# Optimization experiments

Hardware: AMD Instinct MI355X
Metric: run time of the kernel (lower is better)

The kernel has to match this reference:

```python
import jax, jax.numpy as jnp
import numpy as np

TEMPERATURE = 0.07
EPS = 1e-8


def setup_inputs() -> dict:
    key = jax.random.key(0)
    k1, k2 = jax.random.split(key)
    B, D = 8192, 256
    embeddings = jax.random.normal(k1, (B, D), dtype=jnp.float32)
    labels = jax.random.randint(k2, (B,), 0, 6, dtype=jnp.int64)
    return {"embeddings": embeddings, "labels": labels}


def reference(embeddings, labels):
    B = embeddings.shape[0]
    # F.normalize(p=2, dim=1): x / max(||x||, eps)
    norm = jnp.linalg.norm(embeddings, axis=1, keepdims=True)
    en = embeddings / jnp.maximum(norm, 1e-12)
    sim = en @ en.T  # [B, B]
    s = sim / TEMPERATURE

    eye = jnp.eye(B, dtype=bool)
    same = labels[:, None] == labels[None, :]
    pos_mask = same & ~eye            # [B, B]
    neg_mask = (~same) & ~eye         # [B, B]

    exp_s = jnp.exp(s)
    # per-row sum of exp over negatives (matches inner-loop denominator term)
    neg_sum = jnp.sum(jnp.where(neg_mask, exp_s, 0.0), axis=1)  # [B]

    # rows contribute only if they have >=1 positive AND >=1 negative
    row_valid = (pos_mask.sum(axis=1) > 0) & (neg_mask.sum(axis=1) > 0)
    pair_mask = pos_mask & row_valid[:, None]

    # -log( exp(s_ij) / (exp(s_ij) + neg_sum_i + 1e-8) ) per positive pair
    per_pair = -jnp.log(exp_s / (exp_s + neg_sum[:, None] + EPS))
    total = jnp.sum(jnp.where(pair_mask, per_pair, 0.0))
    count = jnp.sum(pair_mask)
    loss = jnp.where(count > 0, total / jnp.maximum(count, 1).astype(total.dtype), 0.0)
    return loss
```

## Files before the change

### kernel.cpp

```cpp
#include <hip/hip_runtime.h>
#include <hip/hip_bf16.h>

#define B_ 8192
#define D_ 256
#define TINV 14.285714285714285f
#define EPS_ 1e-8f
#define BK 32
#define NBLK 32
#define NT 64
#define NTRI (NT*(NT+1)/2)

typedef short short8 __attribute__((ext_vector_type(8)));
typedef float f32x4 __attribute__((ext_vector_type(4)));

__device__ __forceinline__ void mfma_bf16(f32x4& acc, short8 a, short8 b) {
    asm("v_mfma_f32_16x16x32_bf16 %0, %1, %2, %0" : "+v"(acc) : "v"(a), "v"(b));
}

__device__ __forceinline__ void mfma_fence() {
    __builtin_amdgcn_sched_barrier(0);
    asm volatile("s_nop 7\ns_nop 7" ::);
}

__device__ __forceinline__ unsigned short f2bf(float x) {
    __hip_bfloat16 h = __float2bfloat16(x);
    return __builtin_bit_cast(unsigned short, h);
}

__device__ __forceinline__ void tri_decode(int idx, int& bi, int& bj) {
    int t = NTRI - 1 - idx;
    int u = (int)((sqrtf(8.f * (float)t + 1.f) - 1.f) * 0.5f);
    while (u * (u + 1) / 2 > t) --u;
    while ((u + 1) * (u + 2) / 2 <= t) ++u;
    bi = (NT - 1) - u;
    bj = (NT - 1) - (t - u * (u + 1) / 2);
}

__device__ __forceinline__ void stage(const char* gbase, int row0, int k0,
                                      short* ldst, int lane, int wid) {
    int p = (wid << 6) + lane;
    int row = p >> 2;
    int kb = (p & 3) ^ ((row >> 1) & 3);
    const char* g = gbase + ((size_t)(row0 + row) * (D_ * 2) + (size_t)(k0 + kb * 8) * 2);
    __builtin_amdgcn_global_load_lds(
        (const __attribute__((address_space(1))) unsigned int*)g,
        (__attribute__((address_space(3))) unsigned int*)(ldst + ((size_t)wid << 9)),
        16, 0, 0);
}

__device__ __forceinline__ void compute_step(const short* lA, const short* lB,
                                             int lane, int wm, int wn, f32x4 acc[2][4]) {
    int rl = lane & 15, kb = lane >> 4;
    short8 a[2];
#pragma unroll
    for (int m = 0; m < 2; ++m) {
        int row = wm * 32 + m * 16 + rl;
        a[m] = ((const short8*)lA)[row * 4 + (kb ^ ((row >> 1) & 3))];
    }
#pragma unroll
    for (int n = 0; n < 4; ++n) {
        int row = wn * 64 + n * 16 + rl;
        short8 b = ((const short8*)lB)[row * 4 + (kb ^ ((row >> 1) & 3))];
        mfma_bf16(acc[0][n], a[0], b);
        mfma_bf16(acc[1][n], a[1], b);
    }
}

__device__ __forceinline__ void gemm_pipe(const char* enb, int i0, int j0,
                                          short (*lA)[128 * BK], short (*lB)[128 * BK],
                                          int lane, int wid, int wm, int wn,
                                          f32x4 acc[2][4]) {
    stage(enb, i0, 0, lA[0], lane, wid);
    stage(enb, j0, 0, lB[0], lane, wid);
    stage(enb, i0, BK, lA[1], lane, wid);
    stage(enb, j0, BK, lB[1], lane, wid);
#define PIPE_STEP(T, WAITS)                                                     \
    {                                                                           \
        asm volatile(WAITS ::: "memory");                                       \
        __builtin_amdgcn_sched_barrier(0);                                      \
        __builtin_amdgcn_s_barrier();                                           \
        __builtin_amdgcn_sched_barrier(0);                                      \
        if ((T) + 2 < 8) {                                                      \
            stage(enb, i0, ((T) + 2) * BK, lA[((T) + 2) % 3], lane, wid);       \
            stage(enb, j0, ((T) + 2) * BK, lB[((T) + 2) % 3], lane, wid);       \
        }                                                                       \
        compute_step(lA[(T) % 3], lB[(T) % 3], lane, wm, wn, acc);              \
    }
    PIPE_STEP(0, "s_waitcnt vmcnt(2)")
    PIPE_STEP(1, "s_waitcnt vmcnt(2)")
    PIPE_STEP(2, "s_waitcnt vmcnt(2)")
    PIPE_STEP(3, "s_waitcnt vmcnt(2)")
    PIPE_STEP(4, "s_waitcnt vmcnt(2)")
    PIPE_STEP(5, "s_waitcnt vmcnt(2)")
    PIPE_STEP(6, "s_waitcnt vmcnt(2)")
    PIPE_STEP(7, "s_waitcnt vmcnt(0)")
#undef PIPE_STEP
    mfma_fence();
}

__global__ __launch_bounds__(256) void k_bhist(const int* __restrict__ labels,
                                               unsigned* __restrict__ blockhist,
                                               float* __restrict__ negsum,
                                               float* __restrict__ total) {
    __shared__ unsigned h[8];
    int b = blockIdx.x, t = threadIdx.x;
    if (t < 8) h[t] = 0;
    negsum[b * 256 + t] = 0.f;
    if (b == 0 && t == 0) *total = 0.f;
    __syncthreads();
    atomicAdd(&h[labels[b * 256 + t] & 7], 1u);
    __syncthreads();
    if (t < 8) blockhist[b * 8 + t] = h[t];
}

__global__ __launch_bounds__(256) void k_pos(const int* __restrict__ labels,
                                             const unsigned* __restrict__ blockhist,
                                             unsigned* __restrict__ hist,
                                             int* __restrict__ pos) {
    __shared__ unsigned cnt[8][NBLK];
    __shared__ unsigned clsbase[8];
    __shared__ unsigned wcnt[4][8];
    int b = blockIdx.x, t = threadIdx.x;
    { int bb = t >> 3, c = t & 7; cnt[c][bb] = blockhist[bb * 8 + c]; }
    __syncthreads();
    if (t < 8) {
        unsigned run = 0;
        for (int b2 = 0; b2 < NBLK; ++b2) {
            unsigned v = cnt[t][b2];
            cnt[t][b2] = run;
            run += v;
        }
        clsbase[t] = run;
        if (b == 0) hist[t] = run;
    }
    __syncthreads();
    if (t == 0) {
        unsigned run = 0;
        for (int c = 0; c < 8; ++c) {
            unsigned tot = clsbase[c];
            clsbase[c] = run;
            run += tot;
        }
    }
    __syncthreads();
    int row = b * 256 + t;
    int c = labels[row] & 7;
    int lane = t & 63, w = t >> 6;
    unsigned long long lanebelow = (1ull << lane) - 1ull;
    unsigned myrank = 0;
#pragma unroll
    for (int cv = 0; cv < 8; ++cv) {
        unsigned long long mask = __ballot(c == cv);
        if (lane == 0) wcnt[w][cv] = (unsigned)__popcll(mask);
        if (c == cv) myrank = (unsigned)__popcll(mask & lanebelow);
    }
    __syncthreads();
    unsigned pre = 0;
    for (int wp = 0; wp < 4; ++wp) if (wp < w) pre += wcnt[wp][c];
    pos[row] = (int)(clsbase[c] + cnt[c][b] + pre + myrank);
}

__global__ __launch_bounds__(256) void k_scatter(const float* __restrict__ emb,
                                                 const int* __restrict__ labels,
                                                 const int* __restrict__ pos,
                                                 __hip_bfloat16* __restrict__ en_s,
                                                 int* __restrict__ lab_s) {
    int row = blockIdx.x * 4 + (threadIdx.x >> 6);
    int lane = threadIdx.x & 63;
    float4 v = reinterpret_cast<const float4*>(emb)[(size_t)row * 64 + lane];
    float ss = v.x * v.x + v.y * v.y + v.z * v.z + v.w * v.w;
#pragma unroll
    for (int off = 32; off >= 1; off >>= 1) ss += __shfl_xor(ss, off, 64);
    float scale = 1.0f / fmaxf(sqrtf(ss), 1e-12f);
    int p = pos[row];
    ushort4 o;
    o.x = f2bf(v.x * scale);
    o.y = f2bf(v.y * scale);
    o.z = f2bf(v.z * scale);
    o.w = f2bf(v.w * scale);
    reinterpret_cast<ushort4*>(en_s)[(size_t)p * 64 + lane] = o;
    if (lane == 0) lab_s[p] = labels[row] & 7;
}

template <bool USEP>
__global__ __launch_bounds__(512, 8) void k_negsum(const __hip_bfloat16* __restrict__ en,
                                                   const int* __restrict__ lab_s,
                                                   float* __restrict__ P,
                                                   float* __restrict__ negsum) {
    __shared__ short lA[3][128 * BK];
    __shared__ short lB[3][128 * BK];
    __shared__ int sLi[128], sLj[128];
    int bi, bj;
    tri_decode(blockIdx.x, bi, bj);
    int i0 = bi * 128, j0 = bj * 128;
    int tid = threadIdx.x;
    if (tid < 128) sLi[tid] = lab_s[i0 + tid];
    else if (tid < 256) sLj[tid - 128] = lab_s[j0 + tid - 128];
    __syncthreads();

    int lane = tid & 63, wid = tid >> 6;
    int wm = wid >> 1, wn = wid & 1;
    f32x4 acc[2][4] = {};
    gemm_pipe((const char*)en, i0, j0, lA, lB, lane, wid, wm, wn, acc);

    int rl = lane & 15, rowg = (lane >> 4) * 4;
    int lj[4], li[2][4];
#pragma unroll
    for (int n = 0; n < 4; ++n) lj[n] = sLj[wn * 64 + n * 16 + rl];
#pragma unroll
    for (int m = 0; m < 2; ++m)
#pragma unroll
        for (int r = 0; r < 4; ++r) li[m][r] = sLi[wm * 32 + m * 16 + rowg + r];

    float* sredR = (float*)lA;
    float* sredC = (float*)lB;

    float cp[4] = {0.f, 0.f, 0.f, 0.f};
#pragma unroll
    for (int m = 0; m < 2; ++m) {
        float part[4];
#pragma unroll
        for (int r = 0; r < 4; ++r) {
            part[r] = 0.f;
#pragma unroll
            for (int n = 0; n < 4; ++n) {
                float e = (li[m][r] != lj[n]) ? __expf(acc[m][n][r] * TINV) : 0.f;
                part[r] += e;
                cp[n] += e;
            }
        }
#pragma unroll
        for (int off = 1; off < 16; off <<= 1)
#pragma unroll
            for (int r = 0; r < 4; ++r) part[r] += __shfl_xor(part[r], off, 64);
        if (rl == 0) {
#pragma unroll
            for (int r = 0; r < 4; ++r) {
                int row = wm * 32 + m * 16 + rowg + r;
                if (USEP) sredR[wn * 128 + row] = part[r];
                else      atomicAdd(&negsum[i0 + row], part[r]);
            }
        }
    }
    if (bi != bj) {
#pragma unroll
        for (int n = 0; n < 4; ++n) {
            cp[n] += __shfl_xor(cp[n], 16, 64);
            cp[n] += __shfl_xor(cp[n], 32, 64);
            if (lane < 16) {
                int col = wn * 64 + n * 16 + lane;
                if (USEP) sredC[wm * 128 + col] = cp[n];
                else      atomicAdd(&negsum[j0 + col], cp[n]);
            }
        }
    }
    if (USEP) {
        __syncthreads();
        if (tid < 128)
            P[(size_t)bj * B_ + i0 + tid] = sredR[tid] + sredR[128 + tid];
        else if (tid < 256 && bi != bj) {
            int c = tid - 128;
            P[(size_t)bi * B_ + j0 + c] =
                sredC[c] + sredC[128 + c] + sredC[256 + c] + sredC[384 + c];
        }
    }
}

__global__ __launch_bounds__(256) void k_red(const float* __restrict__ P,
                                             float* __restrict__ negsum) {
    int i = blockIdx.x * 256 + threadIdx.x;
    float s = 0.f;
#pragma unroll 8
    for (int k = 0; k < 64; ++k) s += P[(size_t)k * B_ + i];
    negsum[i] = s;
}

__global__ __launch_bounds__(512, 8) void k_pairs(const __hip_bfloat16* __restrict__ en,
                                                  const int* __restrict__ lab_s,
                                                  const float* __restrict__ negsum,
                                                  const unsigned* __restrict__ hist,
                                                  float* __restrict__ total) {
    int bi, bj;
    tri_decode(blockIdx.x, bi, bj);
    int i0 = bi * 128, j0 = bj * 128;
    if (lab_s[j0] > lab_s[i0 + 127]) return;

    __shared__ short lA[3][128 * BK];
    __shared__ short lB[3][128 * BK];
    __shared__ int sLi[128], sLj[128];
    __shared__ float sNgI[128], sNgJ[128];
    int tid = threadIdx.x;
    if (tid < 128) {
        int l = lab_s[i0 + tid];
        unsigned h = hist[l];
        sLi[tid] = (h > 1u && h < (unsigned)B_) ? l : -1;
        sNgI[tid] = negsum[i0 + tid] + EPS_;
    } else if (tid < 256) {
        int idx = tid - 128;
        int l = lab_s[j0 + idx];
        unsigned h = hist[l];
        sLj[idx] = (h > 1u && h < (unsigned)B_) ? l : -1;
        sNgJ[idx] = negsum[j0 + idx] + EPS_;
    }
    __syncthreads();

    int lane = tid & 63, wid = tid >> 6;
    int wm = wid >> 1, wn = wid & 1;
    f32x4 acc[2][4] = {};
    gemm_pipe((const char*)en, i0, j0, lA, lB, lane, wid, wm, wn, acc);

    int rl = lane & 15, rowg = (lane >> 4) * 4;
    int lj[4];
    float ngJ[4];
#pragma unroll
    for (int n = 0; n < 4; ++n) {
        lj[n] = sLj[wn * 64 + n * 16 + rl];
        ngJ[n] = sNgJ[wn * 64 + n * 16 + rl];
    }

    bool offd = (bi != bj);
    float tot = 0.f;
#pragma unroll
    for (int m = 0; m < 2; ++m) {
#pragma unroll
        for (int r = 0; r < 4; ++r) {
            int ii = wm * 32 + m * 16 + rowg + r;
            int li = sLi[ii];
            float ngI = sNgI[ii];
#pragma unroll
            for (int n = 0; n < 4; ++n) {
                int jj = wn * 64 + n * 16 + rl;
                bool use = (li == lj[n]) && (li >= 0) && (offd || ii != jj);
                if (use) {
                    float s = acc[m][n][r] * TINV;
                    float e = __expf(s);
                    float t = __logf(e + ngI) - s;
                    if (offd) t += __logf(e + ngJ[n]) - s;
                    tot += t;
                }
            }
        }
    }
#pragma unroll
    for (int off = 32; off >= 1; off >>= 1) tot += __shfl_xor(tot, off, 64);
    __shared__ float sred[8];
    if (lane == 0) sred[wid] = tot;
    __syncthreads();
    if (tid == 0) {
        float s = 0.f;
#pragma unroll
        for (int w = 0; w < 8; ++w) s += sred[w];
        atomicAdd(total, s);
    }
}

__global__ __launch_bounds__(64) void k_final(const unsigned* __restrict__ hist,
                                              const float* __restrict__ total,
                                              float* __restrict__ out) {
    int t = threadIdx.x;
    unsigned c = 0;
    if (t < 8) {
        unsigned h = hist[t];
        if (h > 1u && h < (unsigned)B_) c = h * (h - 1u);
    }
#pragma unroll
    for (int off = 4; off >= 1; off >>= 1) c += (unsigned)__shfl_xor((int)c, off, 64);
    if (t == 0) out[0] = (c > 0u) ? total[0] / (float)c : 0.f;
}

extern "C" void kernel_launch(void* const* d_in, const int* in_sizes, int n_in,
                              void* d_out, int out_size, void* d_ws, size_t ws_size,
                              hipStream_t stream) {
    const float* emb = (const float*)d_in[0];
    const int* labels = (const int*)d_in[1];
    float* out = (float*)d_out;
    char* ws = (char*)d_ws;

    const size_t EN_BYTES = (size_t)B_ * D_ * 2;
    __hip_bfloat16* en_s = (__hip_bfloat16*)ws;
    char* p = ws + EN_BYTES;
    float* negsum = (float*)p;            p += (size_t)B_ * 4;
    int* lab_s = (int*)p;                 p += (size_t)B_ * 4;
    int* pos = (int*)p;                   p += (size_t)B_ * 4;
    unsigned* blockhist = (unsigned*)p;   p += NBLK * 8 * 4;
    unsigned* hist = (unsigned*)p;        p += 64;
    float* total = (float*)p;             p += 64;
    float* P = (float*)p;
    size_t need = (size_t)(p - ws) + (size_t)NT * B_ * 4;
    bool bigws = ws_size >= need;

    k_bhist<<<NBLK, 256, 0, stream>>>(labels, blockhist, negsum, total);
    k_pos<<<NBLK, 256, 0, stream>>>(labels, blockhist, hist, pos);
    k_scatter<<<B_ / 4, 256, 0, stream>>>(emb, labels, pos, en_s, lab_s);
    if (bigws) {
        k_negsum<true><<<NTRI, 512, 0, stream>>>(en_s, lab_s, P, negsum);
        k_red<<<B_ / 256, 256, 0, stream>>>(P, negsum);
    } else {
        k_negsum<false><<<NTRI, 512, 0, stream>>>(en_s, lab_s, P, negsum);
    }
    k_pairs<<<NTRI, 512, 0, stream>>>(en_s, lab_s, negsum, hist, total);
    k_final<<<1, 64, 0, stream>>>(hist, total, out);
}
```

Measured before the change: 73.12 us.

## Use atomic negsum accumulation, drop partial buffer and reduction kernel

Removes the per-tile partial-sum buffer P and the separate k_red reduction kernel, so k_negsum always accumulates row and column negative sums into negsum with global atomicAdd. The label staging through shared memory and its __syncthreads are removed; labels are now loaded straight from global memory and those loads are placed before the last pipeline step to hide their latency. This saves one kernel launch, the P round trip and a block barrier, but adds atomic contention on negsum and makes the float summation order nondeterministic.

```diff
diff --git a/kernel.cpp b/kernel.cpp
--- a/kernel.cpp
+++ b/kernel.cpp
@@ -66,14 +66,6 @@
     }
 }
 
-__device__ __forceinline__ void gemm_pipe(const char* enb, int i0, int j0,
-                                          short (*lA)[128 * BK], short (*lB)[128 * BK],
-                                          int lane, int wid, int wm, int wn,
-                                          f32x4 acc[2][4]) {
-    stage(enb, i0, 0, lA[0], lane, wid);
-    stage(enb, j0, 0, lB[0], lane, wid);
-    stage(enb, i0, BK, lA[1], lane, wid);
-    stage(enb, j0, BK, lB[1], lane, wid);
 #define PIPE_STEP(T, WAITS)                                                     \
     {                                                                           \
         asm volatile(WAITS ::: "memory");                                       \
@@ -86,6 +78,15 @@
         }                                                                       \
         compute_step(lA[(T) % 3], lB[(T) % 3], lane, wm, wn, acc);              \
     }
+
+__device__ __forceinline__ void gemm_pipe(const char* enb, int i0, int j0,
+                                          short (*lA)[128 * BK], short (*lB)[128 * BK],
+                                          int lane, int wid, int wm, int wn,
+                                          f32x4 acc[2][4]) {
+    stage(enb, i0, 0, lA[0], lane, wid);
+    stage(enb, j0, 0, lB[0], lane, wid);
+    stage(enb, i0, BK, lA[1], lane, wid);
+    stage(enb, j0, BK, lB[1], lane, wid);
     PIPE_STEP(0, "s_waitcnt vmcnt(2)")
     PIPE_STEP(1, "s_waitcnt vmcnt(2)")
     PIPE_STEP(2, "s_waitcnt vmcnt(2)")
@@ -94,7 +95,6 @@
     PIPE_STEP(5, "s_waitcnt vmcnt(2)")
     PIPE_STEP(6, "s_waitcnt vmcnt(2)")
     PIPE_STEP(7, "s_waitcnt vmcnt(0)")
-#undef PIPE_STEP
     mfma_fence();
 }
 
@@ -182,38 +182,41 @@
     if (lane == 0) lab_s[p] = labels[row] & 7;
 }
 
-template <bool USEP>
 __global__ __launch_bounds__(512, 8) void k_negsum(const __hip_bfloat16* __restrict__ en,
                                                    const int* __restrict__ lab_s,
-                                                   float* __restrict__ P,
                                                    float* __restrict__ negsum) {
     __shared__ short lA[3][128 * BK];
     __shared__ short lB[3][128 * BK];
-    __shared__ int sLi[128], sLj[128];
     int bi, bj;
     tri_decode(blockIdx.x, bi, bj);
     int i0 = bi * 128, j0 = bj * 128;
     int tid = threadIdx.x;
-    if (tid < 128) sLi[tid] = lab_s[i0 + tid];
-    else if (tid < 256) sLj[tid - 128] = lab_s[j0 + tid - 128];
-    __syncthreads();
-
     int lane = tid & 63, wid = tid >> 6;
     int wm = wid >> 1, wn = wid & 1;
+    int rl = lane & 15, rowg = (lane >> 4) * 4;
+    const char* enb = (const char*)en;
+
     f32x4 acc[2][4] = {};
-    gemm_pipe((const char*)en, i0, j0, lA, lB, lane, wid, wm, wn, acc);
-
-    int rl = lane & 15, rowg = (lane >> 4) * 4;
+    stage(enb, i0, 0, lA[0], lane, wid);
+    stage(enb, j0, 0, lB[0], lane, wid);
+    stage(enb, i0, BK, lA[1], lane, wid);
+    stage(enb, j0, BK, lB[1], lane, wid);
+    PIPE_STEP(0, "s_waitcnt vmcnt(2)")
+    PIPE_STEP(1, "s_waitcnt vmcnt(2)")
+    PIPE_STEP(2, "s_waitcnt vmcnt(2)")
+    PIPE_STEP(3, "s_waitcnt vmcnt(2)")
+    PIPE_STEP(4, "s_waitcnt vmcnt(2)")
+    PIPE_STEP(5, "s_waitcnt vmcnt(2)")
+    PIPE_STEP(6, "s_waitcnt vmcnt(2)")
     int lj[4], li[2][4];
 #pragma unroll
-    for (int n = 0; n < 4; ++n) lj[n] = sLj[wn * 64 + n * 16 + rl];
+    for (int n = 0; n < 4; ++n) lj[n] = lab_s[j0 + wn * 64 + n * 16 + rl];
 #pragma unroll
     for (int m = 0; m < 2; ++m)
 #pragma unroll
-        for (int r = 0; r < 4; ++r) li[m][r] = sLi[wm * 32 + m * 16 + rowg + r];
-
-    float* sredR = (float*)lA;
-    float* sredC = (float*)lB;
+        for (int r = 0; r < 4; ++r) li[m][r] = lab_s[i0 + wm * 32 + m * 16 + rowg + r];
+    PIPE_STEP(7, "s_waitcnt vmcnt(0)")
+    mfma_fence();
 
     float cp[4] = {0.f, 0.f, 0.f, 0.f};
 #pragma unroll
@@ -235,11 +238,8 @@
             for (int r = 0; r < 4; ++r) part[r] += __shfl_xor(part[r], off, 64);
         if (rl == 0) {
 #pragma unroll
-            for (int r = 0; r < 4; ++r) {
-                int row = wm * 32 + m * 16 + rowg + r;
-                if (USEP) sredR[wn * 128 + row] = part[r];
-                else      atomicAdd(&negsum[i0 + row], part[r]);
-            }
+            for (int r = 0; r < 4; ++r)
+                atomicAdd(&negsum[i0 + wm * 32 + m * 16 + rowg + r], part[r]);
         }
     }
     if (bi != bj) {
@@ -247,32 +247,10 @@
         for (int n = 0; n < 4; ++n) {
             cp[n] += __shfl_xor(cp[n], 16, 64);
             cp[n] += __shfl_xor(cp[n], 32, 64);
-            if (lane < 16) {
-                int col = wn * 64 + n * 16 + lane;
-                if (USEP) sredC[wm * 128 + col] = cp[n];
-                else      atomicAdd(&negsum[j0 + col], cp[n]);
-            }
-        }
-    }
-    if (USEP) {
-        __syncthreads();
-        if (tid < 128)
-            P[(size_t)bj * B_ + i0 + tid] = sredR[tid] + sredR[128 + tid];
-        else if (tid < 256 && bi != bj) {
-            int c = tid - 128;
-            P[(size_t)bi * B_ + j0 + c] =
-                sredC[c] + sredC[128 + c] + sredC[256 + c] + sredC[384 + c];
-        }
-    }
-}
-
-__global__ __launch_bounds__(256) void k_red(const float* __restrict__ P,
-                                             float* __restrict__ negsum) {
-    int i = blockIdx.x * 256 + threadIdx.x;
-    float s = 0.f;
-#pragma unroll 8
-    for (int k = 0; k < 64; ++k) s += P[(size_t)k * B_ + i];
-    negsum[i] = s;
+            if (lane < 16)
+                atomicAdd(&negsum[j0 + wn * 64 + n * 16 + lane], cp[n]);
+        }
+    }
 }
 
 __global__ __launch_bounds__(512, 8) void k_pairs(const __hip_bfloat16* __restrict__ en,
@@ -385,19 +363,11 @@
     unsigned* blockhist = (unsigned*)p;   p += NBLK * 8 * 4;
     unsigned* hist = (unsigned*)p;        p += 64;
     float* total = (float*)p;             p += 64;
-    float* P = (float*)p;
-    size_t need = (size_t)(p - ws) + (size_t)NT * B_ * 4;
-    bool bigws = ws_size >= need;
 
     k_bhist<<<NBLK, 256, 0, stream>>>(labels, blockhist, negsum, total);
     k_pos<<<NBLK, 256, 0, stream>>>(labels, blockhist, hist, pos);
     k_scatter<<<B_ / 4, 256, 0, stream>>>(emb, labels, pos, en_s, lab_s);
-    if (bigws) {
-        k_negsum<true><<<NTRI, 512, 0, stream>>>(en_s, lab_s, P, negsum);
-        k_red<<<B_ / 256, 256, 0, stream>>>(P, negsum);
-    } else {
-        k_negsum<false><<<NTRI, 512, 0, stream>>>(en_s, lab_s, P, negsum);
-    }
+    k_negsum<<<NTRI, 512, 0, stream>>>(en_s, lab_s, negsum);
     k_pairs<<<NTRI, 512, 0, stream>>>(en_s, lab_s, negsum, hist, total);
     k_final<<<1, 64, 0, stream>>>(hist, total, out);
 }
```

Result: slower. 82.15 us (+12.4%).
